# Optimization experiments

Measured on AMD Instinct MI355X. Metric: run time of the kernel, lower is better.

The kernel has to match this reference:

```python
import jax, jax.numpy as jnp
import numpy as np

DIM = 384
FRACTION = 16   # quant_bits=16 -> fixed-point fraction bits
INTEGER = 16
WEIGHT_BITS = 5
SHIFT_MIN = -(2 ** (WEIGHT_BITS - 1) - 2)  # -14 (DeepShift shift_range for 5-bit)


def _ste(x, qx):
    # straight-through estimator: forward qx, backward identity
    return x + jax.lax.stop_gradient(qx - x)


def _clampabs(w, mn, mx):
    # clamp |w| into [mn, mx], preserving sign (zeros stay zero)
    return jnp.sign(w) * jnp.clip(jnp.abs(w), mn, mx)


def _round_power_of_2(w):
    # w -> sign(w) * 2^round(log2(|w|))
    shift = jnp.round(jnp.log2(jnp.maximum(jnp.abs(w), 1e-30)))
    return jnp.sign(w) * jnp.exp2(shift)


def _round_to_fixed(x, fraction=FRACTION, integer=INTEGER):
    delta = 2.0 ** (-fraction)
    bound = 2.0 ** (integer - 1)
    return jnp.clip(jnp.floor(x / delta) * delta, -bound, bound - 1)


def setup_inputs() -> dict:
    key = jax.random.key(0)
    k1, k2, k3 = jax.random.split(key, 3)
    x = jax.random.normal(k1, (32, DIM, 56, 56), dtype=jnp.float32)
    weight = jax.random.normal(k2, (DIM, 1, 3, 3), dtype=jnp.float32) * 0.1
    bias = jax.random.normal(k3, (DIM,), dtype=jnp.float32) * 0.01
    return {"x": x, "weight": weight, "bias": bias}


def reference(x, weight, bias):
    # weight: clamp magnitude to [2^-14, 2^0], then round to signed power of two (5-bit shift)
    w = _ste(weight, _clampabs(weight, 2.0 ** SHIFT_MIN, 1.0))
    w = _ste(w, _round_power_of_2(w))
    # activations / bias: 16-bit fixed-point rounding
    xq = _ste(x, _round_to_fixed(x))
    bq = _ste(bias, _round_to_fixed(bias))
    # depthwise 3x3 conv, stride 1, padding 1, groups = DIM
    out = jax.lax.conv_general_dilated(
        xq, w,
        window_strides=(1, 1),
        padding=((1, 1), (1, 1)),
        feature_group_count=DIM,
        dimension_numbers=("NCHW", "OIHW", "NCHW"),
    )
    return out + bq[None, :, None, None]
```

## Files before the change

### kernel.cpp

```cpp
#include <hip/hip_runtime.h>


#define DW_C   384
#define DW_H   56
#define DW_W   56
#define DW_HW  3136
#define NW4    14

__device__ __forceinline__ float qfix(float v) {
    v = floorf(v * 65536.0f) * (1.0f / 65536.0f);
    return fminf(fmaxf(v, -32768.0f), 32767.0f);
}

struct Row { float l, a, b, c, d, r; };

__global__ __launch_bounds__(256) void quant_wb(
    const float* __restrict__ wgt, const float* __restrict__ bias,
    float* __restrict__ wq, float* __restrict__ bq)
{
    int i = blockIdx.x * 256 + threadIdx.x;
    if (i < DW_C * 9) {
        float wv = wgt[i];
        float aw = fabsf(wv);
        float cw = fminf(fmaxf(aw, 6.103515625e-05f ), 1.0f);
        float q  = exp2f(rintf(log2f(cw)));
        wq[i] = (wv > 0.0f) ? q : ((wv < 0.0f) ? -q : 0.0f);
    }
    if (i < DW_C) bq[i] = qfix(bias[i]);
}

template<bool PRE>
__global__ __launch_bounds__(256, 8) void peg_shift_stream(
    const float* __restrict__ x, const float* __restrict__ wgt,
    const float* __restrict__ bias, float* __restrict__ out,
    const float* __restrict__ wsq, const float* __restrict__ wsb,
    int ntask)
{
    const int task = blockIdx.x * 256 + threadIdx.x;
    if (task >= ntask) return;

    const int plane = task / 42;
    const int t42   = task - plane * 42;
    const int seg   = t42 / NW4;
    const int w4    = t42 - seg * NW4;
    const int c     = plane % DW_C;
    const int r0    = seg * 19;
    const int n     = (seg == 2) ? 18 : 19;
    const int rlim  = min(r0 + n + 1, DW_H);

    const bool hl = (w4 > 0);
    const bool hr = (w4 < NW4 - 1);

    float ww[9];
    float bqv;
    if (PRE) {
        const float* wp = wsq + c * 9;
#pragma unroll
        for (int t = 0; t < 9; ++t) ww[t] = wp[t];
        bqv = wsb[c];
    } else {
        const float* wp = wgt + c * 9;
#pragma unroll
        for (int t = 0; t < 9; ++t) {
            float wv = wp[t];
            float aw = fabsf(wv);
            float cw = fminf(fmaxf(aw, 6.103515625e-05f), 1.0f);
            float q  = exp2f(rintf(log2f(cw)));
            ww[t] = (wv > 0.0f) ? q : ((wv < 0.0f) ? -q : 0.0f);
        }
        bqv = qfix(bias[c]);
    }

    const float* xb = x + (size_t)plane * DW_HW + w4 * 4;

    auto loadraw = [&](int rr, float4& m, float& lv, float& rv) {
        m.x = m.y = m.z = m.w = 0.0f; lv = 0.0f; rv = 0.0f;
        if (rr >= 0 && rr < rlim) {
            const float* p = xb + rr * DW_W;
            m = *(const float4*)p;
            if (hl) lv = p[-1];
            if (hr) rv = p[4];
        }
    };
    auto quant = [&](const float4& m, float lv, float rv) -> Row {
        Row q;
        q.l = qfix(lv);  q.a = qfix(m.x); q.b = qfix(m.y);
        q.c = qfix(m.z); q.d = qfix(m.w); q.r = qfix(rv);
        return q;
    };

    float4 m0, m1, m2, mP, mQ;
    float  l0, r0v, l1, r1v, l2, r2v, lP, rP, lQ, rQ;
    loadraw(r0 - 1, m0, l0, r0v);
    loadraw(r0,     m1, l1, r1v);
    loadraw(r0 + 1, m2, l2, r2v);
    loadraw(r0 + 2, mP, lP, rP);
    Row A = quant(m0, l0, r0v);
    Row B = quant(m1, l1, r1v);
    Row C = quant(m2, l2, r2v);

    float* ob = out + (size_t)plane * DW_HW + r0 * DW_W + w4 * 4;

    for (int i = 0; i < n; ++i) {
        loadraw(r0 + i + 3, mQ, lQ, rQ);

        float o0 = bqv, o1 = bqv, o2 = bqv, o3 = bqv;
        o0 = fmaf(A.l, ww[0], fmaf(A.a, ww[1], fmaf(A.b, ww[2], o0)));
        o1 = fmaf(A.a, ww[0], fmaf(A.b, ww[1], fmaf(A.c, ww[2], o1)));
        o2 = fmaf(A.b, ww[0], fmaf(A.c, ww[1], fmaf(A.d, ww[2], o2)));
        o3 = fmaf(A.c, ww[0], fmaf(A.d, ww[1], fmaf(A.r, ww[2], o3)));
        o0 = fmaf(B.l, ww[3], fmaf(B.a, ww[4], fmaf(B.b, ww[5], o0)));
        o1 = fmaf(B.a, ww[3], fmaf(B.b, ww[4], fmaf(B.c, ww[5], o1)));
        o2 = fmaf(B.b, ww[3], fmaf(B.c, ww[4], fmaf(B.d, ww[5], o2)));
        o3 = fmaf(B.c, ww[3], fmaf(B.d, ww[4], fmaf(B.r, ww[5], o3)));
        o0 = fmaf(C.l, ww[6], fmaf(C.a, ww[7], fmaf(C.b, ww[8], o0)));
        o1 = fmaf(C.a, ww[6], fmaf(C.b, ww[7], fmaf(C.c, ww[8], o1)));
        o2 = fmaf(C.b, ww[6], fmaf(C.c, ww[7], fmaf(C.d, ww[8], o2)));
        o3 = fmaf(C.c, ww[6], fmaf(C.d, ww[7], fmaf(C.r, ww[8], o3)));

        float4 ov; ov.x = o0; ov.y = o1; ov.z = o2; ov.w = o3;
        *(float4*)ob = ov;
        ob += DW_W;

        A = B; B = C;
        C = quant(mP, lP, rP);
        mP = mQ; lP = lQ; rP = rQ;
    }
}

extern "C" void kernel_launch(void* const* d_in, const int* in_sizes, int n_in,
                              void* d_out, int out_size, void* d_ws, size_t ws_size,
                              hipStream_t stream) {
    const float* x = (const float*)d_in[0];
    const float* w = (const float*)d_in[1];
    const float* b = (const float*)d_in[2];
    float* out = (float*)d_out;

    int planes  = in_sizes[0] / DW_HW;
    int tasks   = planes * 42;
    int nblocks = (tasks + 255) / 256;

    size_t need = (size_t)(DW_C * 9 + DW_C) * sizeof(float);
    if (d_ws && ws_size >= need) {
        float* wq = (float*)d_ws;
        float* bq = wq + DW_C * 9;
        quant_wb<<<(DW_C * 9 + 255) / 256, 256, 0, stream>>>(w, b, wq, bq);
        peg_shift_stream<true><<<nblocks, 256, 0, stream>>>(x, w, b, out, wq, bq, tasks);
    } else {
        peg_shift_stream<false><<<nblocks, 256, 0, stream>>>(x, w, b, out, nullptr, nullptr, tasks);
    }
}
```

Baseline: 330.5 us.

## Stage each quantized plane in swizzled LDS and compute 4x4 output tiles per thread

Measured after the change: 270.9 us. 1.22x faster.

```diff
diff --git a/kernel.cpp b/kernel.cpp
--- a/kernel.cpp
+++ b/kernel.cpp
@@ -6,13 +6,25 @@
 #define DW_W   56
 #define DW_HW  3136
 #define NW4    14
+#define ROWS_L 58
+#define STRIDE 68
+#define LDS_DW (ROWS_L * STRIDE)
 
 __device__ __forceinline__ float qfix(float v) {
     v = floorf(v * 65536.0f) * (1.0f / 65536.0f);
     return fminf(fmaxf(v, -32768.0f), 32767.0f);
 }
 
-struct Row { float l, a, b, c, d, r; };
+__device__ __forceinline__ float4 qfix4(float4 v) {
+    v.x = qfix(v.x); v.y = qfix(v.y); v.z = qfix(v.z); v.w = qfix(v.w);
+    return v;
+}
+
+__device__ __forceinline__ int swz(int r, int d) {
+    return r * STRIDE + (d ^ (((r >> 2) & 3) << 3));
+}
+
+struct RowW { float l, a, b, cN, d, r; };
 
 __global__ __launch_bounds__(256) void quant_wb(
     const float* __restrict__ wgt, const float* __restrict__ bias,
@@ -30,36 +42,52 @@
 }
 
 template<bool PRE>
-__global__ __launch_bounds__(256, 8) void peg_shift_stream(
+__global__ __launch_bounds__(256) void peg_shift_v8(
     const float* __restrict__ x, const float* __restrict__ wgt,
     const float* __restrict__ bias, float* __restrict__ out,
-    const float* __restrict__ wsq, const float* __restrict__ wsb,
-    int ntask)
+    const float* __restrict__ wsq, const float* __restrict__ wsb)
 {
-    const int task = blockIdx.x * 256 + threadIdx.x;
-    if (task >= ntask) return;
+    __shared__ float sm[LDS_DW];
 
-    const int plane = task / 42;
-    const int t42   = task - plane * 42;
-    const int seg   = t42 / NW4;
-    const int w4    = t42 - seg * NW4;
-    const int c     = plane % DW_C;
-    const int r0    = seg * 19;
-    const int n     = (seg == 2) ? 18 : 19;
-    const int rlim  = min(r0 + n + 1, DW_H);
+    const int tid   = threadIdx.x;
+    const int plane = blockIdx.x;
+    const int ch    = plane % DW_C;
 
-    const bool hl = (w4 > 0);
-    const bool hr = (w4 < NW4 - 1);
+    if (tid < 2 * STRIDE) {
+        int r = (tid < STRIDE) ? 0 : (ROWS_L - 1);
+        sm[r * STRIDE + (tid % STRIDE)] = 0.0f;
+    }
+    {
+        int i = tid;
+        if (i < 112) {
+            int r = 1 + (i >> 1);
+            int d = (i & 1) ? 60 : 3;
+            sm[swz(r, d)] = 0.0f;
+        }
+    }
 
-    float ww[9];
-    float bqv;
+    {
+        const float4* x4 = (const float4*)(x + (size_t)plane * DW_HW);
+#pragma unroll
+        for (int j = 0; j < 4; ++j) {
+            int s_ = tid + j * 256;
+            if (s_ < 784) {
+                float4 v = x4[s_];
+                int r  = 1 + s_ / NW4;
+                int cc = s_ - (s_ / NW4) * NW4;
+                *(float4*)&sm[swz(r, 4 + 4 * cc)] = qfix4(v);
+            }
+        }
+    }
+
+    float ww[9], bqv;
     if (PRE) {
-        const float* wp = wsq + c * 9;
+        const float* wp = wsq + ch * 9;
 #pragma unroll
         for (int t = 0; t < 9; ++t) ww[t] = wp[t];
-        bqv = wsb[c];
+        bqv = wsb[ch];
     } else {
-        const float* wp = wgt + c * 9;
+        const float* wp = wgt + ch * 9;
 #pragma unroll
         for (int t = 0; t < 9; ++t) {
             float wv = wp[t];
@@ -68,63 +96,52 @@
             float q  = exp2f(rintf(log2f(cw)));
             ww[t] = (wv > 0.0f) ? q : ((wv < 0.0f) ? -q : 0.0f);
         }
-        bqv = qfix(bias[c]);
+        bqv = qfix(bias[ch]);
     }
 
-    const float* xb = x + (size_t)plane * DW_HW + w4 * 4;
+    __syncthreads();
 
-    auto loadraw = [&](int rr, float4& m, float& lv, float& rv) {
-        m.x = m.y = m.z = m.w = 0.0f; lv = 0.0f; rv = 0.0f;
-        if (rr >= 0 && rr < rlim) {
-            const float* p = xb + rr * DW_W;
-            m = *(const float4*)p;
-            if (hl) lv = p[-1];
-            if (hr) rv = p[4];
+    if (tid < 196) {
+        const int g  = tid / NW4;
+        const int cc = tid - g * NW4;
+        const int dl = 3 + 4 * cc, dm = 4 + 4 * cc, dr = 8 + 4 * cc;
+
+        auto ldrow = [&](int rl) -> RowW {
+            RowW R;
+            R.l = sm[swz(rl, dl)];
+            float4 m = *(const float4*)&sm[swz(rl, dm)];
+            R.a = m.x; R.b = m.y; R.cN = m.z; R.d = m.w;
+            R.r = sm[swz(rl, dr)];
+            return R;
+        };
+
+        RowW A = ldrow(4 * g);
+        RowW B = ldrow(4 * g + 1);
+        RowW C = ldrow(4 * g + 2);
+
+        float* op = out + (size_t)plane * DW_HW + (4 * g) * DW_W + 4 * cc;
+
+#define ROWF(RW, W0, W1, W2)                                            \
+        o0 = fmaf(RW.l,  W0, fmaf(RW.a,  W1, fmaf(RW.b,  W2, o0)));     \
+        o1 = fmaf(RW.a,  W0, fmaf(RW.b,  W1, fmaf(RW.cN, W2, o1)));     \
+        o2 = fmaf(RW.b,  W0, fmaf(RW.cN, W1, fmaf(RW.d,  W2, o2)));     \
+        o3 = fmaf(RW.cN, W0, fmaf(RW.d,  W1, fmaf(RW.r,  W2, o3)));
+
+#pragma unroll
+        for (int i = 0; i < 4; ++i) {
+            float o0 = bqv, o1 = bqv, o2 = bqv, o3 = bqv;
+            ROWF(A, ww[0], ww[1], ww[2])
+            ROWF(B, ww[3], ww[4], ww[5])
+            ROWF(C, ww[6], ww[7], ww[8])
+            float4 ov; ov.x = o0; ov.y = o1; ov.z = o2; ov.w = o3;
+            *(float4*)op = ov;
+            op += DW_W;
+            if (i < 3) {
+                A = B; B = C;
+                C = ldrow(4 * g + 3 + i);
+            }
         }
-    };
-    auto quant = [&](const float4& m, float lv, float rv) -> Row {
-        Row q;
-        q.l = qfix(lv);  q.a = qfix(m.x); q.b = qfix(m.y);
-        q.c = qfix(m.z); q.d = qfix(m.w); q.r = qfix(rv);
-        return q;
-    };
-
-    float4 m0, m1, m2, mP, mQ;
-    float  l0, r0v, l1, r1v, l2, r2v, lP, rP, lQ, rQ;
-    loadraw(r0 - 1, m0, l0, r0v);
-    loadraw(r0,     m1, l1, r1v);
-    loadraw(r0 + 1, m2, l2, r2v);
-    loadraw(r0 + 2, mP, lP, rP);
-    Row A = quant(m0, l0, r0v);
-    Row B = quant(m1, l1, r1v);
-    Row C = quant(m2, l2, r2v);
-
-    float* ob = out + (size_t)plane * DW_HW + r0 * DW_W + w4 * 4;
-
-    for (int i = 0; i < n; ++i) {
-        loadraw(r0 + i + 3, mQ, lQ, rQ);
-
-        float o0 = bqv, o1 = bqv, o2 = bqv, o3 = bqv;
-        o0 = fmaf(A.l, ww[0], fmaf(A.a, ww[1], fmaf(A.b, ww[2], o0)));
-        o1 = fmaf(A.a, ww[0], fmaf(A.b, ww[1], fmaf(A.c, ww[2], o1)));
-        o2 = fmaf(A.b, ww[0], fmaf(A.c, ww[1], fmaf(A.d, ww[2], o2)));
-        o3 = fmaf(A.c, ww[0], fmaf(A.d, ww[1], fmaf(A.r, ww[2], o3)));
-        o0 = fmaf(B.l, ww[3], fmaf(B.a, ww[4], fmaf(B.b, ww[5], o0)));
-        o1 = fmaf(B.a, ww[3], fmaf(B.b, ww[4], fmaf(B.c, ww[5], o1)));
-        o2 = fmaf(B.b, ww[3], fmaf(B.c, ww[4], fmaf(B.d, ww[5], o2)));
-        o3 = fmaf(B.c, ww[3], fmaf(B.d, ww[4], fmaf(B.r, ww[5], o3)));
-        o0 = fmaf(C.l, ww[6], fmaf(C.a, ww[7], fmaf(C.b, ww[8], o0)));
-        o1 = fmaf(C.a, ww[6], fmaf(C.b, ww[7], fmaf(C.c, ww[8], o1)));
-        o2 = fmaf(C.b, ww[6], fmaf(C.c, ww[7], fmaf(C.d, ww[8], o2)));
-        o3 = fmaf(C.c, ww[6], fmaf(C.d, ww[7], fmaf(C.r, ww[8], o3)));
-
-        float4 ov; ov.x = o0; ov.y = o1; ov.z = o2; ov.w = o3;
-        *(float4*)ob = ov;
-        ob += DW_W;
-
-        A = B; B = C;
-        C = quant(mP, lP, rP);
-        mP = mQ; lP = lQ; rP = rQ;
+#undef ROWF
     }
 }
 
@@ -136,17 +153,15 @@
     const float* b = (const float*)d_in[2];
     float* out = (float*)d_out;
 
-    int planes  = in_sizes[0] / DW_HW;
-    int tasks   = planes * 42;
-    int nblocks = (tasks + 255) / 256;
+    int planes = in_sizes[0] / DW_HW;
 
     size_t need = (size_t)(DW_C * 9 + DW_C) * sizeof(float);
     if (d_ws && ws_size >= need) {
         float* wq = (float*)d_ws;
         float* bq = wq + DW_C * 9;
         quant_wb<<<(DW_C * 9 + 255) / 256, 256, 0, stream>>>(w, b, wq, bq);
-        peg_shift_stream<true><<<nblocks, 256, 0, stream>>>(x, w, b, out, wq, bq, tasks);
+        peg_shift_v8<true><<<planes, 256, 0, stream>>>(x, w, b, out, wq, bq);
     } else {
-        peg_shift_stream<false><<<nblocks, 256, 0, stream>>>(x, w, b, out, nullptr, nullptr, tasks);
+        peg_shift_v8<false><<<planes, 256, 0, stream>>>(x, w, b, out, nullptr, nullptr);
     }
 }
```

## Map one plane per wave and exchange row halos with lane shuffles

Applied to the files above, without the earlier changes.

Result: faster. 294.7 us (-10.8%).

```diff
diff --git a/kernel.cpp b/kernel.cpp
--- a/kernel.cpp
+++ b/kernel.cpp
@@ -5,14 +5,13 @@
 #define DW_H   56
 #define DW_W   56
 #define DW_HW  3136
-#define NW4    14
 
 __device__ __forceinline__ float qfix(float v) {
     v = floorf(v * 65536.0f) * (1.0f / 65536.0f);
     return fminf(fmaxf(v, -32768.0f), 32767.0f);
 }
 
-struct Row { float l, a, b, c, d, r; };
+struct RowQ { float l, a, b, c, d, r; };
 
 __global__ __launch_bounds__(256) void quant_wb(
     const float* __restrict__ wgt, const float* __restrict__ bias,
@@ -30,29 +29,25 @@
 }
 
 template<bool PRE>
-__global__ __launch_bounds__(256, 8) void peg_shift_stream(
+__global__ __launch_bounds__(256, 8) void peg_shift_v9(
     const float* __restrict__ x, const float* __restrict__ wgt,
     const float* __restrict__ bias, float* __restrict__ out,
-    const float* __restrict__ wsq, const float* __restrict__ wsb,
-    int ntask)
+    const float* __restrict__ wsq, const float* __restrict__ wsb)
 {
-    const int task = blockIdx.x * 256 + threadIdx.x;
-    if (task >= ntask) return;
+    const int tid   = threadIdx.x;
+    const int wave  = tid >> 6;
+    const int lane  = tid & 63;
+    const int g     = lane >> 4;
+    const int j     = lane & 15;
+    const int plane = blockIdx.x * 4 + wave;
+    const int c     = plane % DW_C;
+    const int rb    = g * 14;
+    const int rlim  = min(rb + 15, DW_H);
 
-    const int plane = task / 42;
-    const int t42   = task - plane * 42;
-    const int seg   = t42 / NW4;
-    const int w4    = t42 - seg * NW4;
-    const int c     = plane % DW_C;
-    const int r0    = seg * 19;
-    const int n     = (seg == 2) ? 18 : 19;
-    const int rlim  = min(r0 + n + 1, DW_H);
+    const bool act  = (j < 14);
+    const int  jc   = act ? j : 13;
 
-    const bool hl = (w4 > 0);
-    const bool hr = (w4 < NW4 - 1);
-
-    float ww[9];
-    float bqv;
+    float ww[9], bqv;
     if (PRE) {
         const float* wp = wsq + c * 9;
 #pragma unroll
@@ -71,61 +66,57 @@
         bqv = qfix(bias[c]);
     }
 
-    const float* xb = x + (size_t)plane * DW_HW + w4 * 4;
+    const float* xb = x + (size_t)plane * DW_HW + jc * 4;
 
-    auto loadraw = [&](int rr, float4& m, float& lv, float& rv) {
-        m.x = m.y = m.z = m.w = 0.0f; lv = 0.0f; rv = 0.0f;
-        if (rr >= 0 && rr < rlim) {
-            const float* p = xb + rr * DW_W;
-            m = *(const float4*)p;
-            if (hl) lv = p[-1];
-            if (hr) rv = p[4];
-        }
+    auto loadraw = [&](int rr) -> float4 {
+        float4 m; m.x = m.y = m.z = m.w = 0.0f;
+        if (rr >= 0 && rr < rlim) m = *(const float4*)(xb + rr * DW_W);
+        return m;
     };
-    auto quant = [&](const float4& m, float lv, float rv) -> Row {
-        Row q;
-        q.l = qfix(lv);  q.a = qfix(m.x); q.b = qfix(m.y);
-        q.c = qfix(m.z); q.d = qfix(m.w); q.r = qfix(rv);
+
+    auto mkrow = [&](float4 m) -> RowQ {
+        RowQ q;
+        q.a = qfix(m.x); q.b = qfix(m.y); q.c = qfix(m.z); q.d = qfix(m.w);
+        float lu = __shfl_up(q.d, 1);
+        float rd = __shfl_down(q.a, 1);
+        q.l = (j == 0)  ? 0.0f : lu;
+        q.r = (j >= 13) ? 0.0f : rd;
         return q;
     };
 
-    float4 m0, m1, m2, mP, mQ;
-    float  l0, r0v, l1, r1v, l2, r2v, lP, rP, lQ, rQ;
-    loadraw(r0 - 1, m0, l0, r0v);
-    loadraw(r0,     m1, l1, r1v);
-    loadraw(r0 + 1, m2, l2, r2v);
-    loadraw(r0 + 2, mP, lP, rP);
-    Row A = quant(m0, l0, r0v);
-    Row B = quant(m1, l1, r1v);
-    Row C = quant(m2, l2, r2v);
+    float4 mP = loadraw(rb + 2);
+    RowQ A = mkrow(loadraw(rb - 1));
+    RowQ B = mkrow(loadraw(rb));
+    RowQ C = mkrow(loadraw(rb + 1));
 
-    float* ob = out + (size_t)plane * DW_HW + r0 * DW_W + w4 * 4;
+    float* ob = out + (size_t)plane * DW_HW + rb * DW_W + j * 4;
 
-    for (int i = 0; i < n; ++i) {
-        loadraw(r0 + i + 3, mQ, lQ, rQ);
+#define ROWF(RW, W0, W1, W2)                                          \
+    o0 = fmaf(RW.l, W0, fmaf(RW.a, W1, fmaf(RW.b, W2, o0)));          \
+    o1 = fmaf(RW.a, W0, fmaf(RW.b, W1, fmaf(RW.c, W2, o1)));          \
+    o2 = fmaf(RW.b, W0, fmaf(RW.c, W1, fmaf(RW.d, W2, o2)));          \
+    o3 = fmaf(RW.c, W0, fmaf(RW.d, W1, fmaf(RW.r, W2, o3)));
+
+#pragma unroll
+    for (int i = 0; i < 14; ++i) {
+        float4 mQ = loadraw(rb + i + 3);
 
         float o0 = bqv, o1 = bqv, o2 = bqv, o3 = bqv;
-        o0 = fmaf(A.l, ww[0], fmaf(A.a, ww[1], fmaf(A.b, ww[2], o0)));
-        o1 = fmaf(A.a, ww[0], fmaf(A.b, ww[1], fmaf(A.c, ww[2], o1)));
-        o2 = fmaf(A.b, ww[0], fmaf(A.c, ww[1], fmaf(A.d, ww[2], o2)));
-        o3 = fmaf(A.c, ww[0], fmaf(A.d, ww[1], fmaf(A.r, ww[2], o3)));
-        o0 = fmaf(B.l, ww[3], fmaf(B.a, ww[4], fmaf(B.b, ww[5], o0)));
-        o1 = fmaf(B.a, ww[3], fmaf(B.b, ww[4], fmaf(B.c, ww[5], o1)));
-        o2 = fmaf(B.b, ww[3], fmaf(B.c, ww[4], fmaf(B.d, ww[5], o2)));
-        o3 = fmaf(B.c, ww[3], fmaf(B.d, ww[4], fmaf(B.r, ww[5], o3)));
-        o0 = fmaf(C.l, ww[6], fmaf(C.a, ww[7], fmaf(C.b, ww[8], o0)));
-        o1 = fmaf(C.a, ww[6], fmaf(C.b, ww[7], fmaf(C.c, ww[8], o1)));
-        o2 = fmaf(C.b, ww[6], fmaf(C.c, ww[7], fmaf(C.d, ww[8], o2)));
-        o3 = fmaf(C.c, ww[6], fmaf(C.d, ww[7], fmaf(C.r, ww[8], o3)));
+        ROWF(A, ww[0], ww[1], ww[2])
+        ROWF(B, ww[3], ww[4], ww[5])
+        ROWF(C, ww[6], ww[7], ww[8])
 
-        float4 ov; ov.x = o0; ov.y = o1; ov.z = o2; ov.w = o3;
-        *(float4*)ob = ov;
+        if (act) {
+            float4 ov; ov.x = o0; ov.y = o1; ov.z = o2; ov.w = o3;
+            *(float4*)ob = ov;
+        }
         ob += DW_W;
 
         A = B; B = C;
-        C = quant(mP, lP, rP);
-        mP = mQ; lP = lQ; rP = rQ;
+        C = mkrow(mP);
+        mP = mQ;
     }
+#undef ROWF
 }
 
 extern "C" void kernel_launch(void* const* d_in, const int* in_sizes, int n_in,
@@ -137,16 +128,15 @@
     float* out = (float*)d_out;
 
     int planes  = in_sizes[0] / DW_HW;
-    int tasks   = planes * 42;
-    int nblocks = (tasks + 255) / 256;
+    int nblocks = planes / 4;
 
     size_t need = (size_t)(DW_C * 9 + DW_C) * sizeof(float);
     if (d_ws && ws_size >= need) {
         float* wq = (float*)d_ws;
         float* bq = wq + DW_C * 9;
         quant_wb<<<(DW_C * 9 + 255) / 256, 256, 0, stream>>>(w, b, wq, bq);
-        peg_shift_stream<true><<<nblocks, 256, 0, stream>>>(x, w, b, out, wq, bq, tasks);
+        peg_shift_v9<true><<<nblocks, 256, 0, stream>>>(x, w, b, out, wq, bq);
     } else {
-        peg_shift_stream<false><<<nblocks, 256, 0, stream>>>(x, w, b, out, nullptr, nullptr, tasks);
+        peg_shift_v9<false><<<nblocks, 256, 0, stream>>>(x, w, b, out, nullptr, nullptr);
     }
 }
```
